# Optimization experiments

Measured on AMD Instinct MI355X. Metric: run time of the kernel, lower is better.

Reference implementation:

```python
import jax, jax.numpy as jnp
import numpy as np

B, N, E, H, P = 4, 512, 512, 32, 128
D = E // H
SCALING = D ** -0.5
EPS = 1e-5


def layer_norm(x, g, b):
    mu = jnp.mean(x, axis=-1, keepdims=True)
    var = jnp.var(x, axis=-1, keepdims=True)
    return (x - mu) * jax.lax.rsqrt(var + EPS) * g + b


def setup_inputs() -> dict:
    key = jax.random.key(0)
    ks = jax.random.split(key, 12)
    inp = {
        "query": jax.random.normal(ks[0], (B, N, E), jnp.float32),
        "pair": jax.random.normal(ks[1], (B, N, N, P), jnp.float32),
        "attn_mask": jnp.zeros((B, H, N, N), jnp.float32),
        "delta_pos": jax.random.normal(ks[2], (B, N, N, 3), jnp.float32),
        # parameters
        "ln_g": jnp.ones((E,), jnp.float32),
        "ln_b": jnp.zeros((E,), jnp.float32),
        "Wq": jax.random.normal(ks[3], (E, E), jnp.float32) * (1.0 / np.sqrt(E)),
        "Wk": jax.random.normal(ks[4], (E, E), jnp.float32) * (1.0 / np.sqrt(E)),
        "Wv": jax.random.normal(ks[5], (E, E), jnp.float32) * (1.0 / np.sqrt(E)),
        "pln_g": jnp.ones((P,), jnp.float32),
        "pln_b": jnp.zeros((P,), jnp.float32),
        "Wb": jax.random.normal(ks[6], (H, P), jnp.float32) * (1.0 / np.sqrt(P)),
        "bb": jnp.zeros((H,), jnp.float32),
        "Wf": jax.random.normal(ks[7], (1, E), jnp.float32) * (1.0 / np.sqrt(E)),
    }
    return inp


def reference(query, pair, attn_mask, delta_pos,
              ln_g, ln_b, Wq, Wk, Wv, pln_g, pln_b, Wb, bb, Wf):
    x = layer_norm(query, ln_g, ln_b)                       # (B,N,E)
    q = (x @ Wq.T).reshape(B, N, H, D).transpose(0, 2, 1, 3) * SCALING  # (B,H,N,D)
    k = (x @ Wk.T).reshape(B, N, H, D).transpose(0, 2, 1, 3)
    v = (x @ Wv.T).reshape(B, N, H, D).transpose(0, 2, 1, 3)
    attn = jnp.einsum('bhid,bhjd->bhij', q, k)              # (B,H,N,N)
    pair_n = layer_norm(pair, pln_g, pln_b)
    bias = (pair_n @ Wb.T + bb).transpose(0, 3, 1, 2)       # (B,H,N,N)
    attn = jax.nn.softmax(attn + bias + attn_mask, axis=-1)  # dropout off (eval)
    # rot_attn_probs: attn (B,H,N,N) * delta_pos (B,N,N,3) -> contract over j with v
    # out per (b, i, coord c, head h, d): sum_j attn[b,h,i,j]*delta_pos[b,i,j,c]*v[b,h,j,d]
    xo = jnp.einsum('bhij,bijc,bhjd->bichd', attn, delta_pos, v)  # (B,N,3,H,D)
    xo = xo.reshape(B, N, 3, E)
    cur_force = (xo @ Wf.T).reshape(B, N, 3)
    return cur_force
```

## Files before the change

### kernel.cpp

```cpp
#include <hip/hip_runtime.h>
#include <hip/hip_bf16.h>
#include <stdint.h>

constexpr int cB = 4, cN = 512, cE = 512, cH = 32, cP = 128;

typedef __attribute__((ext_vector_type(8))) short bf16x8;
typedef __attribute__((ext_vector_type(4))) float f32x4;

__device__ __forceinline__ unsigned short f2bf(float f) {
    union { float f; unsigned u; } v; v.f = f;
    unsigned u = v.u;
    u += 0x7fffu + ((u >> 16) & 1u);
    return (unsigned short)(u >> 16);
}
__device__ __forceinline__ float bf2f(unsigned short s) {
    union { unsigned u; float f; } v; v.u = ((unsigned)s) << 16;
    return v.f;
}

__global__ __launch_bounds__(256) void ln_query_kernel(
    const float* __restrict__ q, const float* __restrict__ g,
    const float* __restrict__ b, float* __restrict__ xn)
{
    int row = blockIdx.x;
    int t = threadIdx.x;
    const float* xr = q + (size_t)row * cE;
    float2 v = *(const float2*)(xr + t * 2);
    float s = v.x + v.y;
    float ss = v.x * v.x + v.y * v.y;
    #pragma unroll
    for (int o = 32; o > 0; o >>= 1) {
        s  += __shfl_down(s, o, 64);
        ss += __shfl_down(ss, o, 64);
    }
    __shared__ float red[8];
    int wv = t >> 6, ln = t & 63;
    if (ln == 0) { red[wv] = s; red[wv + 4] = ss; }
    __syncthreads();
    if (t == 0) {
        float S = red[0] + red[1] + red[2] + red[3];
        float SS = red[4] + red[5] + red[6] + red[7];
        float mu = S * (1.0f / cE);
        float var = SS * (1.0f / cE) - mu * mu;
        red[0] = mu; red[1] = rsqrtf(var + 1e-5f);
    }
    __syncthreads();
    float mu = red[0], rs = red[1];
    float2 gg = *(const float2*)(g + t * 2);
    float2 bb2 = *(const float2*)(b + t * 2);
    float2 o2;
    o2.x = (v.x - mu) * rs * gg.x + bb2.x;
    o2.y = (v.y - mu) * rs * gg.y + bb2.y;
    *(float2*)(xn + (size_t)row * cE + t * 2) = o2;
}

__global__ void setup_kernel(
    const float* __restrict__ Wb, const float* __restrict__ pg,
    const float* __restrict__ pb, const float* __restrict__ bbv,
    unsigned short* __restrict__ Wbp, float* __restrict__ Sh,
    float* __restrict__ cbh)
{
    int h = threadIdx.x;
    if (h < cH) {
        float s = 0.f, c = bbv[h];
        for (int p = 0; p < cP; ++p) {
            float wv = Wb[h * cP + p];
            float wp = wv * pg[p];
            s += wp;
            c += pb[p] * wv;
            Wbp[h * cP + p] = f2bf(wp);
        }
        Sh[h] = s; cbh[h] = c;
    }
}

__global__ __launch_bounds__(64) void qkv_kernel(
    const float* __restrict__ xn,
    const float* __restrict__ Wq, const float* __restrict__ Wk,
    const float* __restrict__ Wv, const float* __restrict__ Wf,
    float* __restrict__ Q, float* __restrict__ K, float* __restrict__ w)
{
    int mtile = blockIdx.x & 31;
    int ntile = blockIdx.x >> 5;
    int mat = ntile >> 3;
    int ncol0 = (ntile & 7) * 64;
    const float* W = (mat == 0) ? Wq : ((mat == 1) ? Wk : Wv);
    int rm = mtile * 64;
    int t = threadIdx.x;
    int tm = t >> 3, tn = t & 7;

    __shared__ float As[32][68];
    __shared__ float Bs[32][68];
    float acc[8][8];
    #pragma unroll
    for (int i = 0; i < 8; ++i)
        #pragma unroll
        for (int j = 0; j < 8; ++j) acc[i][j] = 0.f;

    for (int k0 = 0; k0 < cE; k0 += 32) {
        #pragma unroll
        for (int s = 0; s < 8; ++s) {
            int f = t + 64 * s;
            int row = f >> 3, kq = f & 7;
            float4 v = *(const float4*)(xn + (size_t)(rm + row) * cE + k0 + kq * 4);
            As[kq * 4 + 0][row] = v.x; As[kq * 4 + 1][row] = v.y;
            As[kq * 4 + 2][row] = v.z; As[kq * 4 + 3][row] = v.w;
            float4 u = *(const float4*)(W + (size_t)(ncol0 + row) * cE + k0 + kq * 4);
            Bs[kq * 4 + 0][row] = u.x; Bs[kq * 4 + 1][row] = u.y;
            Bs[kq * 4 + 2][row] = u.z; Bs[kq * 4 + 3][row] = u.w;
        }
        __syncthreads();
        #pragma unroll
        for (int kk = 0; kk < 32; ++kk) {
            float a[8], bv[8];
            #pragma unroll
            for (int i = 0; i < 8; ++i) a[i] = As[kk][tm * 8 + i];
            #pragma unroll
            for (int j = 0; j < 8; ++j) bv[j] = Bs[kk][tn * 8 + j];
            #pragma unroll
            for (int i = 0; i < 8; ++i)
                #pragma unroll
                for (int j = 0; j < 8; ++j) acc[i][j] = fmaf(a[i], bv[j], acc[i][j]);
        }
        __syncthreads();
    }

    if (mat < 2) {
        float scale = (mat == 0) ? 0.25f : 1.0f;
        float* dst = (mat == 0) ? Q : K;
        #pragma unroll
        for (int i = 0; i < 8; ++i) {
            int r = rm + tm * 8 + i;
            #pragma unroll
            for (int j = 0; j < 8; ++j)
                dst[(size_t)r * cE + ncol0 + tn * 8 + j] = acc[i][j] * scale;
        }
    } else {
        int col0 = ncol0 + tn * 8;
        int h = col0 >> 4;
        float wf[8];
        #pragma unroll
        for (int j = 0; j < 8; ++j) wf[j] = Wf[col0 + j];
        #pragma unroll
        for (int i = 0; i < 8; ++i) {
            int r = rm + tm * 8 + i;
            float part = 0.f;
            #pragma unroll
            for (int j = 0; j < 8; ++j) part = fmaf(acc[i][j], wf[j], part);
            atomicAdd(&w[(size_t)r * cH + h], part);
        }
    }
}

__global__ __launch_bounds__(256) void attn_kernel(
    const float* __restrict__ pair, const float* __restrict__ mask,
    const float* __restrict__ dpos, const float* __restrict__ Q,
    const float* __restrict__ K, const float* __restrict__ w,
    const unsigned short* __restrict__ Wbp, const float* __restrict__ Sh_g,
    const float* __restrict__ cb_g, float* __restrict__ out)
{
    int bi = blockIdx.x;
    int b = bi >> 9, i = bi & 511;
    int t = threadIdx.x;
    int lane = t & 63, wv = t >> 6;

    __shared__ __align__(16) unsigned short Ap[64 * 136];
    __shared__ __align__(16) unsigned short Bw[32 * 136];
    __shared__ float biasT[64][33];
    __shared__ float qrow[512];
    __shared__ float mrow[64], rrow[64];
    __shared__ float mt[64][33];
    __shared__ float dl[64][4];
    __shared__ float Shs[32], cbs[32];
    __shared__ float statred[64][8];

    {
        const ushort4* src = (const ushort4*)Wbp;
        #pragma unroll
        for (int s = 0; s < 4; ++s) {
            int f = t + 256 * s;
            int hh = f >> 5, p4 = f & 31;
            ushort4 v = src[f];
            *(ushort4*)&Bw[hh * 136 + p4 * 4] = v;
        }
    }
    if (t < 128) {
        float4 qv = *(const float4*)(Q + (size_t)bi * cE + t * 4);
        *(float4*)&qrow[t * 4] = qv;
    }
    if (t < 32) { Shs[t] = Sh_g[t]; cbs[t] = cb_g[t]; }
    __syncthreads();

    int h = t & 31, js = t >> 5;
    float qreg[16];
    #pragma unroll
    for (int d = 0; d < 16; ++d) qreg[d] = qrow[h * 16 + d];
    float Sh_loc = Shs[h], cb_loc = cbs[h];

    float m = -1e30f, l = 0.f, a0 = 0.f, a1 = 0.f, a2 = 0.f;

    const float* pbase = pair + (size_t)bi * cN * cP;
    const float* dbase = dpos + (size_t)bi * cN * 3;
    const float* Kbase = K + (size_t)b * cN * cE;
    const float* wbase = w + (size_t)b * cN * cH;

    for (int j0 = 0; j0 < cN; j0 += 64) {
        #pragma unroll
        for (int s = 0; s < 8; ++s) {
            int f = t + 256 * s;
            int row = f >> 5, c4 = f & 31;
            float4 v = *(const float4*)(pbase + (size_t)(j0 + row) * cP + c4 * 4);
            ushort4 u;
            u.x = f2bf(v.x); u.y = f2bf(v.y); u.z = f2bf(v.z); u.w = f2bf(v.w);
            *(ushort4*)&Ap[row * 136 + c4 * 4] = u;
        }
        #pragma unroll
        for (int s = 0; s < 2; ++s) {
            int f = t + 256 * s;
            int hh = f >> 4, c4 = f & 15;
            float4 v = *(const float4*)(mask + ((size_t)(b * cH + hh) * cN + i) * cN + j0 + c4 * 4);
            mt[c4 * 4 + 0][hh] = v.x; mt[c4 * 4 + 1][hh] = v.y;
            mt[c4 * 4 + 2][hh] = v.z; mt[c4 * 4 + 3][hh] = v.w;
        }
        if (t < 64) {
            const float* dp = dbase + (size_t)(j0 + t) * 3;
            dl[t][0] = dp[0]; dl[t][1] = dp[1]; dl[t][2] = dp[2];
        }
        __syncthreads();

        {
            int r = t >> 2, q = t & 3;
            float s1 = 0.f, s2 = 0.f;
            #pragma unroll
            for (int p = 0; p < 32; ++p) {
                float f = bf2f(Ap[r * 136 + q * 32 + p]);
                s1 += f; s2 = fmaf(f, f, s2);
            }
            statred[r][q] = s1; statred[r][q + 4] = s2;
        }
        __syncthreads();
        if (t < 64) {
            float s1 = statred[t][0] + statred[t][1] + statred[t][2] + statred[t][3];
            float s2 = statred[t][4] + statred[t][5] + statred[t][6] + statred[t][7];
            float mu = s1 * (1.0f / cP);
            float var = s2 * (1.0f / cP) - mu * mu;
            mrow[t] = mu;
            rrow[t] = rsqrtf(var + 1e-5f);
        }
        __syncthreads();

        {
            f32x4 acc0 = {0.f, 0.f, 0.f, 0.f}, acc1 = {0.f, 0.f, 0.f, 0.f};
            int arow = wv * 16 + (lane & 15);
            int kq = (lane >> 4) * 8;
            #pragma unroll
            for (int kb = 0; kb < 4; ++kb) {
                int k = kb * 32 + kq;
                bf16x8 af = *(const bf16x8*)&Ap[arow * 136 + k];
                bf16x8 b0 = *(const bf16x8*)&Bw[(lane & 15) * 136 + k];
                bf16x8 b1 = *(const bf16x8*)&Bw[(16 + (lane & 15)) * 136 + k];
                acc0 = __builtin_amdgcn_mfma_f32_16x16x32_bf16(af, b0, acc0, 0, 0, 0);
                acc1 = __builtin_amdgcn_mfma_f32_16x16x32_bf16(af, b1, acc1, 0, 0, 0);
            }
            int crow = wv * 16 + (lane >> 4) * 4;
            int ccol = lane & 15;
            #pragma unroll
            for (int r = 0; r < 4; ++r) {
                biasT[crow + r][ccol] = acc0[r];
                biasT[crow + r][16 + ccol] = acc1[r];
            }
        }
        __syncthreads();

        #pragma unroll
        for (int jj = 0; jj < 8; ++jj) {
            int jr = js * 8 + jj;
            int j = j0 + jr;
            float bias = rrow[jr] * (biasT[jr][h] - mrow[jr] * Sh_loc) + cb_loc;
            const float4* kp4 = (const float4*)(Kbase + (size_t)j * cE + h * 16);
            float qk = 0.f;
            #pragma unroll
            for (int d4 = 0; d4 < 4; ++d4) {
                float4 kv = kp4[d4];
                qk = fmaf(qreg[d4 * 4 + 0], kv.x, qk);
                qk = fmaf(qreg[d4 * 4 + 1], kv.y, qk);
                qk = fmaf(qreg[d4 * 4 + 2], kv.z, qk);
                qk = fmaf(qreg[d4 * 4 + 3], kv.w, qk);
            }
            float z = qk + bias + mt[jr][h];
            float wj = wbase[(size_t)j * cH + h];
            float mn = fmaxf(m, z);
            float sc = __expf(m - mn);
            float p = __expf(z - mn);
            l = l * sc + p;
            float pw = p * wj;
            a0 = fmaf(pw, dl[jr][0], a0 * sc);
            a1 = fmaf(pw, dl[jr][1], a1 * sc);
            a2 = fmaf(pw, dl[jr][2], a2 * sc);
            m = mn;
        }
        __syncthreads();
    }

    float* red = (float*)mt;
    red[(h * 8 + js) * 6 + 0] = m;
    red[(h * 8 + js) * 6 + 1] = l;
    red[(h * 8 + js) * 6 + 2] = a0;
    red[(h * 8 + js) * 6 + 3] = a1;
    red[(h * 8 + js) * 6 + 4] = a2;
    __syncthreads();
    for (int s = 4; s >= 1; s >>= 1) {
        if (js < s) {
            float* p1 = &red[(h * 8 + js) * 6];
            float* p2 = &red[(h * 8 + js + s) * 6];
            float m1 = p1[0], m2 = p2[0];
            float mn = fmaxf(m1, m2);
            float s1 = __expf(m1 - mn), s2 = __expf(m2 - mn);
            p1[0] = mn;
            p1[1] = p1[1] * s1 + p2[1] * s2;
            p1[2] = p1[2] * s1 + p2[2] * s2;
            p1[3] = p1[3] * s1 + p2[3] * s2;
            p1[4] = p1[4] * s1 + p2[4] * s2;
        }
        __syncthreads();
    }
    if (js == 0) {
        float linv = 1.0f / red[h * 48 + 1];
        biasT[h][0] = red[h * 48 + 2] * linv;
        biasT[h][1] = red[h * 48 + 3] * linv;
        biasT[h][2] = red[h * 48 + 4] * linv;
    }
    __syncthreads();
    if (t < 3) {
        float s = 0.f;
        #pragma unroll
        for (int hh = 0; hh < cH; ++hh) s += biasT[hh][t];
        out[(size_t)bi * 3 + t] = s;
    }
}

extern "C" void kernel_launch(void* const* d_in, const int* in_sizes, int n_in,
                              void* d_out, int out_size, void* d_ws, size_t ws_size,
                              hipStream_t stream)
{
    const float* query = (const float*)d_in[0];
    const float* pair  = (const float*)d_in[1];
    const float* amask = (const float*)d_in[2];
    const float* dpos  = (const float*)d_in[3];
    const float* ln_g  = (const float*)d_in[4];
    const float* ln_b  = (const float*)d_in[5];
    const float* Wq    = (const float*)d_in[6];
    const float* Wk    = (const float*)d_in[7];
    const float* Wv    = (const float*)d_in[8];
    const float* pg    = (const float*)d_in[9];
    const float* pb    = (const float*)d_in[10];
    const float* Wb    = (const float*)d_in[11];
    const float* bbv   = (const float*)d_in[12];
    const float* Wf    = (const float*)d_in[13];
    float* out = (float*)d_out;

    char* ws = (char*)d_ws;
    float* xn = (float*)ws;
    float* Q  = (float*)(ws + (size_t)4 * 1048576);
    float* K  = (float*)(ws + (size_t)8 * 1048576);
    float* w  = (float*)(ws + (size_t)12 * 1048576);
    unsigned short* Wbp = (unsigned short*)(ws + (size_t)12 * 1048576 + 262144);
    float* Sh  = (float*)(ws + (size_t)12 * 1048576 + 262144 + 8192);
    float* cbh = (float*)(ws + (size_t)12 * 1048576 + 262144 + 8192 + 128);

    ln_query_kernel<<<cB * cN, 256, 0, stream>>>(query, ln_g, ln_b, xn);
    setup_kernel<<<1, 64, 0, stream>>>(Wb, pg, pb, bbv, Wbp, Sh, cbh);
    hipMemsetAsync(w, 0, (size_t)cB * cN * cH * sizeof(float), stream);
    qkv_kernel<<<32 * 24, 64, 0, stream>>>(xn, Wq, Wk, Wv, Wf, Q, K, w);
    attn_kernel<<<cB * cN, 256, 0, stream>>>(pair, amask, dpos, Q, K, w, Wbp, Sh, cbh, out);
}
```

Measured before the change: 960.7 us.

## Prefetch pair tiles into registers and double-buffer attention staging

```diff
diff --git a/kernel.cpp b/kernel.cpp
--- a/kernel.cpp
+++ b/kernel.cpp
@@ -12,10 +12,6 @@
     unsigned u = v.u;
     u += 0x7fffu + ((u >> 16) & 1u);
     return (unsigned short)(u >> 16);
-}
-__device__ __forceinline__ float bf2f(unsigned short s) {
-    union { unsigned u; float f; } v; v.u = ((unsigned)s) << 16;
-    return v.f;
 }
 
 __global__ __launch_bounds__(256) void ln_query_kernel(
@@ -54,27 +50,30 @@
     *(float2*)(xn + (size_t)row * cE + t * 2) = o2;
 }
 
-__global__ void setup_kernel(
+__global__ __launch_bounds__(256) void setup_kernel(
     const float* __restrict__ Wb, const float* __restrict__ pg,
     const float* __restrict__ pb, const float* __restrict__ bbv,
     unsigned short* __restrict__ Wbp, float* __restrict__ Sh,
     float* __restrict__ cbh)
 {
-    int h = threadIdx.x;
-    if (h < cH) {
-        float s = 0.f, c = bbv[h];
-        for (int p = 0; p < cP; ++p) {
-            float wv = Wb[h * cP + p];
-            float wp = wv * pg[p];
-            s += wp;
-            c += pb[p] * wv;
-            Wbp[h * cP + p] = f2bf(wp);
-        }
-        Sh[h] = s; cbh[h] = c;
-    }
-}
-
-__global__ __launch_bounds__(64) void qkv_kernel(
+    int t = threadIdx.x;
+    int h = t >> 3, sub = t & 7;
+    float s = 0.f, c = 0.f;
+    #pragma unroll
+    for (int pp = 0; pp < 16; ++pp) {
+        int p = sub * 16 + pp;
+        float wv = Wb[h * cP + p];
+        float wp = wv * pg[p];
+        s += wp;
+        c = fmaf(pb[p], wv, c);
+        Wbp[h * cP + p] = f2bf(wp);
+    }
+    s += __shfl_xor(s, 1, 64); s += __shfl_xor(s, 2, 64); s += __shfl_xor(s, 4, 64);
+    c += __shfl_xor(c, 1, 64); c += __shfl_xor(c, 2, 64); c += __shfl_xor(c, 4, 64);
+    if (sub == 0) { Sh[h] = s; cbh[h] = c + bbv[h]; }
+}
+
+__global__ __launch_bounds__(256) void qkv_kernel(
     const float* __restrict__ xn,
     const float* __restrict__ Wq, const float* __restrict__ Wk,
     const float* __restrict__ Wv, const float* __restrict__ Wf,
@@ -87,67 +86,74 @@
     const float* W = (mat == 0) ? Wq : ((mat == 1) ? Wk : Wv);
     int rm = mtile * 64;
     int t = threadIdx.x;
-    int tm = t >> 3, tn = t & 7;
+    int tm = t >> 4, tn = t & 15;
 
     __shared__ float As[32][68];
     __shared__ float Bs[32][68];
-    float acc[8][8];
-    #pragma unroll
-    for (int i = 0; i < 8; ++i)
-        #pragma unroll
-        for (int j = 0; j < 8; ++j) acc[i][j] = 0.f;
+    float acc[4][4] = {{0.f}};
+    float4 pa[2], pb2[2];
+
+    auto stage_load = [&](int k0) {
+        #pragma unroll
+        for (int s = 0; s < 2; ++s) {
+            int f = t + 256 * s;
+            int row = f >> 3, kq = f & 7;
+            pa[s]  = *(const float4*)(xn + (size_t)(rm + row) * cE + k0 + kq * 4);
+            pb2[s] = *(const float4*)(W + (size_t)(ncol0 + row) * cE + k0 + kq * 4);
+        }
+    };
+    stage_load(0);
 
     for (int k0 = 0; k0 < cE; k0 += 32) {
-        #pragma unroll
-        for (int s = 0; s < 8; ++s) {
-            int f = t + 64 * s;
+        __syncthreads();
+        #pragma unroll
+        for (int s = 0; s < 2; ++s) {
+            int f = t + 256 * s;
             int row = f >> 3, kq = f & 7;
-            float4 v = *(const float4*)(xn + (size_t)(rm + row) * cE + k0 + kq * 4);
-            As[kq * 4 + 0][row] = v.x; As[kq * 4 + 1][row] = v.y;
-            As[kq * 4 + 2][row] = v.z; As[kq * 4 + 3][row] = v.w;
-            float4 u = *(const float4*)(W + (size_t)(ncol0 + row) * cE + k0 + kq * 4);
-            Bs[kq * 4 + 0][row] = u.x; Bs[kq * 4 + 1][row] = u.y;
-            Bs[kq * 4 + 2][row] = u.z; Bs[kq * 4 + 3][row] = u.w;
+            As[kq * 4 + 0][row] = pa[s].x; As[kq * 4 + 1][row] = pa[s].y;
+            As[kq * 4 + 2][row] = pa[s].z; As[kq * 4 + 3][row] = pa[s].w;
+            Bs[kq * 4 + 0][row] = pb2[s].x; Bs[kq * 4 + 1][row] = pb2[s].y;
+            Bs[kq * 4 + 2][row] = pb2[s].z; Bs[kq * 4 + 3][row] = pb2[s].w;
         }
         __syncthreads();
+        if (k0 + 32 < cE) stage_load(k0 + 32);
         #pragma unroll
         for (int kk = 0; kk < 32; ++kk) {
-            float a[8], bv[8];
-            #pragma unroll
-            for (int i = 0; i < 8; ++i) a[i] = As[kk][tm * 8 + i];
-            #pragma unroll
-            for (int j = 0; j < 8; ++j) bv[j] = Bs[kk][tn * 8 + j];
-            #pragma unroll
-            for (int i = 0; i < 8; ++i)
+            float4 av = *(const float4*)&As[kk][tm * 4];
+            float4 bv = *(const float4*)&Bs[kk][tn * 4];
+            float ar[4] = {av.x, av.y, av.z, av.w};
+            float br[4] = {bv.x, bv.y, bv.z, bv.w};
+            #pragma unroll
+            for (int i2 = 0; i2 < 4; ++i2)
                 #pragma unroll
-                for (int j = 0; j < 8; ++j) acc[i][j] = fmaf(a[i], bv[j], acc[i][j]);
-        }
-        __syncthreads();
+                for (int j2 = 0; j2 < 4; ++j2)
+                    acc[i2][j2] = fmaf(ar[i2], br[j2], acc[i2][j2]);
+        }
     }
 
     if (mat < 2) {
         float scale = (mat == 0) ? 0.25f : 1.0f;
         float* dst = (mat == 0) ? Q : K;
         #pragma unroll
-        for (int i = 0; i < 8; ++i) {
-            int r = rm + tm * 8 + i;
-            #pragma unroll
-            for (int j = 0; j < 8; ++j)
-                dst[(size_t)r * cE + ncol0 + tn * 8 + j] = acc[i][j] * scale;
+        for (int i2 = 0; i2 < 4; ++i2) {
+            int r = rm + tm * 4 + i2;
+            #pragma unroll
+            for (int j2 = 0; j2 < 4; ++j2)
+                dst[(size_t)r * cE + ncol0 + tn * 4 + j2] = acc[i2][j2] * scale;
         }
     } else {
-        int col0 = ncol0 + tn * 8;
-        int h = col0 >> 4;
-        float wf[8];
-        #pragma unroll
-        for (int j = 0; j < 8; ++j) wf[j] = Wf[col0 + j];
-        #pragma unroll
-        for (int i = 0; i < 8; ++i) {
-            int r = rm + tm * 8 + i;
+        int col0 = ncol0 + tn * 4;
+        int hh = col0 >> 4;
+        float wf[4];
+        #pragma unroll
+        for (int j2 = 0; j2 < 4; ++j2) wf[j2] = Wf[col0 + j2];
+        #pragma unroll
+        for (int i2 = 0; i2 < 4; ++i2) {
+            int r = rm + tm * 4 + i2;
             float part = 0.f;
             #pragma unroll
-            for (int j = 0; j < 8; ++j) part = fmaf(acc[i][j], wf[j], part);
-            atomicAdd(&w[(size_t)r * cH + h], part);
+            for (int j2 = 0; j2 < 4; ++j2) part = fmaf(acc[i2][j2], wf[j2], part);
+            atomicAdd(&w[(size_t)r * cH + hh], part);
         }
     }
 }
@@ -164,15 +170,13 @@
     int t = threadIdx.x;
     int lane = t & 63, wv = t >> 6;
 
-    __shared__ __align__(16) unsigned short Ap[64 * 136];
     __shared__ __align__(16) unsigned short Bw[32 * 136];
-    __shared__ float biasT[64][33];
+    __shared__ float biasT[2][64][33];
+    __shared__ float mt[2][64][33];
     __shared__ float qrow[512];
-    __shared__ float mrow[64], rrow[64];
-    __shared__ float mt[64][33];
-    __shared__ float dl[64][4];
+    __shared__ float mrow[2][64], rrow[2][64];
+    __shared__ float dl[2][192];
     __shared__ float Shs[32], cbs[32];
-    __shared__ float statred[64][8];
 
     {
         const ushort4* src = (const ushort4*)Wbp;
@@ -189,6 +193,34 @@
         *(float4*)&qrow[t * 4] = qv;
     }
     if (t < 32) { Shs[t] = Sh_g[t]; cbs[t] = cb_g[t]; }
+
+    const float* pbase = pair + (size_t)bi * cN * cP;
+    const float* dbase = dpos + (size_t)bi * cN * 3;
+    const float* Kbase = K + (size_t)b * cN * cE;
+    const float* wbase = w + (size_t)b * cN * cH;
+    const float* mbase = mask + ((size_t)b * cH * cN + i) * cN;
+
+    int arow = wv * 16 + (lane & 15);
+    int kcol = (lane >> 4) * 8;
+
+    float4 pf[8]; float4 mf[2]; float dreg = 0.f;
+    auto loadregs = [&](int j0) {
+        const float* prow = pbase + (size_t)(j0 + arow) * cP + kcol;
+        #pragma unroll
+        for (int kb = 0; kb < 4; ++kb) {
+            pf[2 * kb]     = *(const float4*)(prow + kb * 32);
+            pf[2 * kb + 1] = *(const float4*)(prow + kb * 32 + 4);
+        }
+        #pragma unroll
+        for (int s = 0; s < 2; ++s) {
+            int f = t + 256 * s;
+            int hh = f >> 4, c4 = f & 15;
+            mf[s] = *(const float4*)(mbase + (size_t)hh * cN * cN + j0 + c4 * 4);
+        }
+        if (t < 192) dreg = dbase[j0 * 3 + t];
+    };
+
+    loadregs(0);
     __syncthreads();
 
     int h = t & 31, js = t >> 5;
@@ -199,84 +231,73 @@
 
     float m = -1e30f, l = 0.f, a0 = 0.f, a1 = 0.f, a2 = 0.f;
 
-    const float* pbase = pair + (size_t)bi * cN * cP;
-    const float* dbase = dpos + (size_t)bi * cN * 3;
-    const float* Kbase = K + (size_t)b * cN * cE;
-    const float* wbase = w + (size_t)b * cN * cH;
-
-    for (int j0 = 0; j0 < cN; j0 += 64) {
-        #pragma unroll
-        for (int s = 0; s < 8; ++s) {
-            int f = t + 256 * s;
-            int row = f >> 5, c4 = f & 31;
-            float4 v = *(const float4*)(pbase + (size_t)(j0 + row) * cP + c4 * 4);
-            ushort4 u;
-            u.x = f2bf(v.x); u.y = f2bf(v.y); u.z = f2bf(v.z); u.w = f2bf(v.w);
-            *(ushort4*)&Ap[row * 136 + c4 * 4] = u;
-        }
-        #pragma unroll
-        for (int s = 0; s < 2; ++s) {
-            int f = t + 256 * s;
-            int hh = f >> 4, c4 = f & 15;
-            float4 v = *(const float4*)(mask + ((size_t)(b * cH + hh) * cN + i) * cN + j0 + c4 * 4);
-            mt[c4 * 4 + 0][hh] = v.x; mt[c4 * 4 + 1][hh] = v.y;
-            mt[c4 * 4 + 2][hh] = v.z; mt[c4 * 4 + 3][hh] = v.w;
-        }
-        if (t < 64) {
-            const float* dp = dbase + (size_t)(j0 + t) * 3;
-            dl[t][0] = dp[0]; dl[t][1] = dp[1]; dl[t][2] = dp[2];
-        }
-        __syncthreads();
-
-        {
-            int r = t >> 2, q = t & 3;
-            float s1 = 0.f, s2 = 0.f;
-            #pragma unroll
-            for (int p = 0; p < 32; ++p) {
-                float f = bf2f(Ap[r * 136 + q * 32 + p]);
-                s1 += f; s2 = fmaf(f, f, s2);
-            }
-            statred[r][q] = s1; statred[r][q + 4] = s2;
-        }
-        __syncthreads();
-        if (t < 64) {
-            float s1 = statred[t][0] + statred[t][1] + statred[t][2] + statred[t][3];
-            float s2 = statred[t][4] + statred[t][5] + statred[t][6] + statred[t][7];
+    for (int it = 0; it < 8; ++it) {
+        int cur = it & 1;
+        int j0 = it * 64;
+
+        bf16x8 af[4];
+        float s1 = 0.f, s2 = 0.f;
+        #pragma unroll
+        for (int kb = 0; kb < 4; ++kb) {
+            float4 u0 = pf[2 * kb], u1 = pf[2 * kb + 1];
+            s1 += u0.x + u0.y + u0.z + u0.w + u1.x + u1.y + u1.z + u1.w;
+            s2 = fmaf(u0.x, u0.x, s2); s2 = fmaf(u0.y, u0.y, s2);
+            s2 = fmaf(u0.z, u0.z, s2); s2 = fmaf(u0.w, u0.w, s2);
+            s2 = fmaf(u1.x, u1.x, s2); s2 = fmaf(u1.y, u1.y, s2);
+            s2 = fmaf(u1.z, u1.z, s2); s2 = fmaf(u1.w, u1.w, s2);
+            bf16x8 a;
+            a[0] = (short)f2bf(u0.x); a[1] = (short)f2bf(u0.y);
+            a[2] = (short)f2bf(u0.z); a[3] = (short)f2bf(u0.w);
+            a[4] = (short)f2bf(u1.x); a[5] = (short)f2bf(u1.y);
+            a[6] = (short)f2bf(u1.z); a[7] = (short)f2bf(u1.w);
+            af[kb] = a;
+        }
+        s1 += __shfl_xor(s1, 16, 64); s1 += __shfl_xor(s1, 32, 64);
+        s2 += __shfl_xor(s2, 16, 64); s2 += __shfl_xor(s2, 32, 64);
+        if ((lane >> 4) == 0) {
             float mu = s1 * (1.0f / cP);
             float var = s2 * (1.0f / cP) - mu * mu;
-            mrow[t] = mu;
-            rrow[t] = rsqrtf(var + 1e-5f);
-        }
-        __syncthreads();
-
+            mrow[cur][arow] = mu;
+            rrow[cur][arow] = rsqrtf(var + 1e-5f);
+        }
         {
             f32x4 acc0 = {0.f, 0.f, 0.f, 0.f}, acc1 = {0.f, 0.f, 0.f, 0.f};
-            int arow = wv * 16 + (lane & 15);
-            int kq = (lane >> 4) * 8;
             #pragma unroll
             for (int kb = 0; kb < 4; ++kb) {
-                int k = kb * 32 + kq;
-                bf16x8 af = *(const bf16x8*)&Ap[arow * 136 + k];
+                int k = kb * 32 + kcol;
                 bf16x8 b0 = *(const bf16x8*)&Bw[(lane & 15) * 136 + k];
                 bf16x8 b1 = *(const bf16x8*)&Bw[(16 + (lane & 15)) * 136 + k];
-                acc0 = __builtin_amdgcn_mfma_f32_16x16x32_bf16(af, b0, acc0, 0, 0, 0);
-                acc1 = __builtin_amdgcn_mfma_f32_16x16x32_bf16(af, b1, acc1, 0, 0, 0);
+                acc0 = __builtin_amdgcn_mfma_f32_16x16x32_bf16(af[kb], b0, acc0, 0, 0, 0);
+                acc1 = __builtin_amdgcn_mfma_f32_16x16x32_bf16(af[kb], b1, acc1, 0, 0, 0);
             }
             int crow = wv * 16 + (lane >> 4) * 4;
             int ccol = lane & 15;
             #pragma unroll
             for (int r = 0; r < 4; ++r) {
-                biasT[crow + r][ccol] = acc0[r];
-                biasT[crow + r][16 + ccol] = acc1[r];
+                biasT[cur][crow + r][ccol] = acc0[r];
+                biasT[cur][crow + r][16 + ccol] = acc1[r];
             }
         }
+        #pragma unroll
+        for (int s = 0; s < 2; ++s) {
+            int f = t + 256 * s;
+            int hh = f >> 4, c4 = f & 15;
+            mt[cur][c4 * 4 + 0][hh] = mf[s].x;
+            mt[cur][c4 * 4 + 1][hh] = mf[s].y;
+            mt[cur][c4 * 4 + 2][hh] = mf[s].z;
+            mt[cur][c4 * 4 + 3][hh] = mf[s].w;
+        }
+        if (t < 192) dl[cur][t] = dreg;
+
         __syncthreads();
+
+        if (it < 7) loadregs(j0 + 64);
 
         #pragma unroll
         for (int jj = 0; jj < 8; ++jj) {
             int jr = js * 8 + jj;
             int j = j0 + jr;
-            float bias = rrow[jr] * (biasT[jr][h] - mrow[jr] * Sh_loc) + cb_loc;
+            float bias = rrow[cur][jr] * (biasT[cur][jr][h] - mrow[cur][jr] * Sh_loc) + cb_loc;
             const float4* kp4 = (const float4*)(Kbase + (size_t)j * cE + h * 16);
             float qk = 0.f;
             #pragma unroll
@@ -287,22 +308,21 @@
                 qk = fmaf(qreg[d4 * 4 + 2], kv.z, qk);
                 qk = fmaf(qreg[d4 * 4 + 3], kv.w, qk);
             }
-            float z = qk + bias + mt[jr][h];
+            float z = qk + bias + mt[cur][jr][h];
             float wj = wbase[(size_t)j * cH + h];
             float mn = fmaxf(m, z);
             float sc = __expf(m - mn);
             float p = __expf(z - mn);
             l = l * sc + p;
             float pw = p * wj;
-            a0 = fmaf(pw, dl[jr][0], a0 * sc);
-            a1 = fmaf(pw, dl[jr][1], a1 * sc);
-            a2 = fmaf(pw, dl[jr][2], a2 * sc);
+            a0 = fmaf(pw, dl[cur][jr * 3 + 0], a0 * sc);
+            a1 = fmaf(pw, dl[cur][jr * 3 + 1], a1 * sc);
+            a2 = fmaf(pw, dl[cur][jr * 3 + 2], a2 * sc);
             m = mn;
         }
-        __syncthreads();
-    }
-
-    float* red = (float*)mt;
+    }
+
+    float* red = &mt[0][0][0];
     red[(h * 8 + js) * 6 + 0] = m;
     red[(h * 8 + js) * 6 + 1] = l;
     red[(h * 8 + js) * 6 + 2] = a0;
@@ -315,26 +335,26 @@
             float* p2 = &red[(h * 8 + js + s) * 6];
             float m1 = p1[0], m2 = p2[0];
             float mn = fmaxf(m1, m2);
-            float s1 = __expf(m1 - mn), s2 = __expf(m2 - mn);
+            float e1 = __expf(m1 - mn), e2 = __expf(m2 - mn);
             p1[0] = mn;
-            p1[1] = p1[1] * s1 + p2[1] * s2;
-            p1[2] = p1[2] * s1 + p2[2] * s2;
-            p1[3] = p1[3] * s1 + p2[3] * s2;
-            p1[4] = p1[4] * s1 + p2[4] * s2;
+            p1[1] = p1[1] * e1 + p2[1] * e2;
+            p1[2] = p1[2] * e1 + p2[2] * e2;
+            p1[3] = p1[3] * e1 + p2[3] * e2;
+            p1[4] = p1[4] * e1 + p2[4] * e2;
         }
         __syncthreads();
     }
     if (js == 0) {
         float linv = 1.0f / red[h * 48 + 1];
-        biasT[h][0] = red[h * 48 + 2] * linv;
-        biasT[h][1] = red[h * 48 + 3] * linv;
-        biasT[h][2] = red[h * 48 + 4] * linv;
+        biasT[0][h][0] = red[h * 48 + 2] * linv;
+        biasT[0][h][1] = red[h * 48 + 3] * linv;
+        biasT[0][h][2] = red[h * 48 + 4] * linv;
     }
     __syncthreads();
     if (t < 3) {
         float s = 0.f;
         #pragma unroll
-        for (int hh = 0; hh < cH; ++hh) s += biasT[hh][t];
+        for (int hh = 0; hh < cH; ++hh) s += biasT[0][hh][t];
         out[(size_t)bi * 3 + t] = s;
     }
 }
@@ -369,8 +389,8 @@
     float* cbh = (float*)(ws + (size_t)12 * 1048576 + 262144 + 8192 + 128);
 
     ln_query_kernel<<<cB * cN, 256, 0, stream>>>(query, ln_g, ln_b, xn);
-    setup_kernel<<<1, 64, 0, stream>>>(Wb, pg, pb, bbv, Wbp, Sh, cbh);
+    setup_kernel<<<1, 256, 0, stream>>>(Wb, pg, pb, bbv, Wbp, Sh, cbh);
     hipMemsetAsync(w, 0, (size_t)cB * cN * cH * sizeof(float), stream);
-    qkv_kernel<<<32 * 24, 64, 0, stream>>>(xn, Wq, Wk, Wv, Wf, Q, K, w);
+    qkv_kernel<<<32 * 24, 256, 0, stream>>>(xn, Wq, Wk, Wv, Wf, Q, K, w);
     attn_kernel<<<cB * cN, 256, 0, stream>>>(pair, amask, dpos, Q, K, w, Wbp, Sh, cbh, out);
 }
```

Measured after the change: 994.3 us. 3.5% more time.
